# Kernel tuning notes

Hardware: AMD Instinct MI355X
Metric: run time of the kernel (lower is better)

Reference implementation:

```python
import jax, jax.numpy as jnp
import numpy as np

D_MODEL = 2048
D_INNER = 2 * D_MODEL      # expand=2
D_STATE = 16
D_CONV = 4
DT_RANK = D_MODEL // 16    # ceil(2048/16)=128
BATCH, SEQLEN = 2, 1024


def setup_inputs() -> dict:
    key = jax.random.key(0)
    ks = jax.random.split(key, 10)
    s = 0.02
    inp = {
        "hidden_states": jax.random.normal(ks[0], (BATCH, SEQLEN, D_MODEL), jnp.float32),
        "in_proj_w": jax.random.normal(ks[1], (2 * D_INNER, D_MODEL), jnp.float32) * s,
        "conv_w": jax.random.normal(ks[2], (D_INNER, D_CONV), jnp.float32) * s,
        "conv_b": jax.random.normal(ks[3], (D_INNER,), jnp.float32) * s,
        "x_proj_w": jax.random.normal(ks[4], (DT_RANK + 2 * D_STATE, D_INNER), jnp.float32) * s,
        "dt_proj_w": jax.random.normal(ks[5], (D_INNER, DT_RANK), jnp.float32) * s,
        "dt_proj_b": jax.random.normal(ks[6], (D_INNER,), jnp.float32) * 0.1,
        "A_log": jnp.log(jnp.tile(jnp.arange(1, D_STATE + 1, dtype=jnp.float32), (D_INNER, 1))),
        "D": jnp.ones((D_INNER,), jnp.float32),
        "out_proj_w": jax.random.normal(ks[7], (D_MODEL, D_INNER), jnp.float32) * s,
    }
    return inp


def _mamba_forward(hidden_states, in_proj_w, conv_w, conv_b, x_proj_w,
                   dt_proj_w, dt_proj_b, A_log, D, out_proj_w):
    B, L, _ = hidden_states.shape
    # input projection -> x, z  (each [B, L, D_INNER])
    xz = jnp.einsum('bld,ed->ble', hidden_states, in_proj_w)
    x, z = jnp.split(xz, 2, axis=-1)
    # causal depthwise conv1d (kernel D_CONV) + SiLU
    x_pad = jnp.pad(x, ((0, 0), (D_CONV - 1, 0), (0, 0)))
    windows = jnp.stack([x_pad[:, k:k + L, :] for k in range(D_CONV)], axis=-1)  # [B,L,D,K]
    x_conv = jnp.einsum('bldk,dk->bld', windows, conv_w) + conv_b
    x_act = jax.nn.silu(x_conv)
    # data-dependent SSM parameters
    x_dbl = jnp.einsum('bld,ed->ble', x_act, x_proj_w)
    dt, Bc, Cc = jnp.split(x_dbl, [DT_RANK, DT_RANK + D_STATE], axis=-1)
    dt = jax.nn.softplus(jnp.einsum('blr,dr->bld', dt, dt_proj_w) + dt_proj_b)  # [B,L,D_INNER]
    A = -jnp.exp(A_log)  # [D_INNER, D_STATE]

    # selective scan over time (carry h: [B, D_INNER, D_STATE])
    def step(h, inp):
        x_t, dt_t, B_t, C_t = inp  # [B,D],[B,D],[B,N],[B,N]
        dA = jnp.exp(dt_t[:, :, None] * A[None])          # [B,D,N]
        dBx = dt_t[:, :, None] * B_t[:, None, :] * x_t[:, :, None]
        h = h * dA + dBx
        y = jnp.einsum('bdn,bn->bd', h, C_t)
        return h, y

    xs = (x_act.transpose(1, 0, 2), dt.transpose(1, 0, 2),
          Bc.transpose(1, 0, 2), Cc.transpose(1, 0, 2))
    h0 = jnp.zeros((B, D_INNER, D_STATE), x_act.dtype)
    _, ys = jax.lax.scan(step, h0, xs)          # [L,B,D_INNER]
    y = ys.transpose(1, 0, 2) + x_act * D       # skip connection D*x
    y = y * jax.nn.silu(z)                      # gating
    return jnp.einsum('bld,md->blm', y, out_proj_w)


def reference(hidden_states, in_proj_w, conv_w, conv_b, x_proj_w,
              dt_proj_w, dt_proj_b, A_log, D, out_proj_w):
    return _mamba_forward(hidden_states, in_proj_w, conv_w, conv_b, x_proj_w,
                          dt_proj_w, dt_proj_b, A_log, D, out_proj_w)
```

## Files before the change

### kernel.cpp

```cpp
#include <hip/hip_runtime.h>
#include <cstdint>
#include <cstddef>

#define D_MODEL 2048
#define D_INNER 4096
#define D_IN2   8192
#define D_STATE 16
#define D_CONVK 4
#define DT_RANK 128
#define BATCH   2
#define SEQLEN  1024
#define BL      (BATCH*SEQLEN)
#define XDBL_N  (DT_RANK + 2*D_STATE)
#define XPW_NPAD 256
#define XPROJ_SPLITS 8
#define OUT_SPLITS 2

#define NCHUNK  16
#define LCHUNK  (SEQLEN/NCHUNK)
#define CHW     (BATCH*D_INNER*D_STATE)

#define NB_HID   2048
#define NB_IPW   8192
#define NB_XPW   320
#define NB_XPWZ  192
#define NB_DTW   256
#define NB_OPW   4096
#define NB_XDBLZ 320

typedef short  s8v  __attribute__((ext_vector_type(8)));
typedef float  f4v  __attribute__((ext_vector_type(4)));

__device__ __forceinline__ float softplus_f(float v) {
    return (v > 20.f) ? v : log1pf(__expf(v));
}
__device__ __forceinline__ float silu_f(float v) {
    return v / (1.f + __expf(-v));
}
__device__ __forceinline__ float bf2f(short s) {
    return __uint_as_float(((uint32_t)(uint16_t)s) << 16);
}
__device__ __forceinline__ uint16_t f2bf(float f) {
    uint32_t u = __float_as_uint(f);
    return (uint16_t)((u + 0x7FFFu + ((u >> 16) & 1u)) >> 16);
}
__device__ __forceinline__ uint32_t packbf(float lo, float hi) {
    return ((uint32_t)f2bf(hi) << 16) | (uint32_t)f2bf(lo);
}
__device__ __forceinline__ float quad_sum(float p) {
    p += __int_as_float(__builtin_amdgcn_update_dpp(
            0, __float_as_int(p), 0xB1, 0xF, 0xF, true));
    p += __int_as_float(__builtin_amdgcn_update_dpp(
            0, __float_as_int(p), 0x4E, 0xF, 0xF, true));
    return p;
}

#define GLD16(gp, lp)                                                          \
    __builtin_amdgcn_global_load_lds(                                          \
        (const __attribute__((address_space(1))) void*)(gp),                   \
        (__attribute__((address_space(3))) void*)(lp), 16, 0, 0)

__global__ __launch_bounds__(256)
void k_cast_all(const float* __restrict__ s0, uint32_t* __restrict__ d0,
                const float* __restrict__ s1, uint32_t* __restrict__ d1,
                const float* __restrict__ s2, uint32_t* __restrict__ d2,
                const float* __restrict__ s3, uint32_t* __restrict__ d3,
                const float* __restrict__ s4, uint32_t* __restrict__ d4,
                uint32_t* __restrict__ z0, uint32_t* __restrict__ z1)
{
    int blk = blockIdx.x;
    const float* src = nullptr; uint32_t* dst; int base; int zero = 0;
    if      (blk < NB_HID) { src = s0; dst = d0; base = blk; }
    else if ((blk -= NB_HID)  < NB_IPW)  { src = s1; dst = d1; base = blk; }
    else if ((blk -= NB_IPW)  < NB_XPW)  { src = s2; dst = d2; base = blk; }
    else if ((blk -= NB_XPW)  < NB_XPWZ) { dst = z0; base = blk; zero = 1; }
    else if ((blk -= NB_XPWZ) < NB_DTW)  { src = s3; dst = d3; base = blk; }
    else if ((blk -= NB_DTW)  < NB_OPW)  { src = s4; dst = d4; base = blk; }
    else                                 { dst = z1; base = blk - NB_OPW; zero = 1; }
    const int i = base * 256 + threadIdx.x;
    if (zero) { ((uint4*)dst)[i] = make_uint4(0u, 0u, 0u, 0u); return; }
    const float4 a = ((const float4*)src)[i * 2];
    const float4 b = ((const float4*)src)[i * 2 + 1];
    uint4 o;
    o.x = packbf(a.x, a.y); o.y = packbf(a.z, a.w);
    o.z = packbf(b.x, b.y); o.w = packbf(b.z, b.w);
    ((uint4*)dst)[i] = o;
}

template<int EPI>
__device__ __forceinline__
void gemm_body(const short* __restrict__ A, int lda,
               const short* __restrict__ W, int ldw,
               void* __restrict__ Cv, int ldc, int M, int kchunk)
{
    __shared__ short sA[128 * 64];
    __shared__ short sW[128 * 64];

    const int tid = threadIdx.x;
    const int w   = tid >> 6;
    const int L   = tid & 63;
    const int bm  = blockIdx.y * 128;
    const int bn  = blockIdx.x * 128;
    const int k0  = blockIdx.z * kchunk;

    const int rsub = L >> 3;
    const int c8   = (((L & 7) - rsub) & 7) * 8;
    const short* Ag[4]; const short* Wg[4];
#pragma unroll
    for (int j = 0; j < 4; j++) {
        Ag[j] = A + (size_t)(bm + w * 32 + j * 8 + rsub) * lda + c8 + k0;
        Wg[j] = W + (size_t)(bn + w * 32 + j * 8 + rsub) * ldw + c8 + k0;
    }

    const int wm = (w >> 1) * 64;
    const int wn = (w & 1) * 64;
    const int cl = L & 15;
    const int qd = L >> 4;

    f4v acc[4][4];
#pragma unroll
    for (int i = 0; i < 4; i++)
#pragma unroll
        for (int j = 0; j < 4; j++) acc[i][j] = (f4v){0.f, 0.f, 0.f, 0.f};

    for (int k = 0; k < kchunk; k += 64) {
#pragma unroll
        for (int j = 0; j < 4; j++)
            GLD16(Ag[j] + k, &sA[(w * 32 + j * 8) * 64]);
#pragma unroll
        for (int j = 0; j < 4; j++)
            GLD16(Wg[j] + k, &sW[(w * 32 + j * 8) * 64]);
        __syncthreads();
#pragma unroll
        for (int kk = 0; kk < 2; kk++) {
            const int sl = ((kk * 4 + qd + cl) & 7) * 8;
            s8v a[4], b[4];
#pragma unroll
            for (int mt = 0; mt < 4; mt++)
                a[mt] = *(const s8v*)&sA[(wm + mt * 16 + cl) * 64 + sl];
#pragma unroll
            for (int nt = 0; nt < 4; nt++)
                b[nt] = *(const s8v*)&sW[(wn + nt * 16 + cl) * 64 + sl];
#pragma unroll
            for (int mt = 0; mt < 4; mt++)
#pragma unroll
                for (int nt = 0; nt < 4; nt++)
                    acc[mt][nt] = __builtin_amdgcn_mfma_f32_16x16x32_bf16(
                        a[mt], b[nt], acc[mt][nt], 0, 0, 0);
        }
        __syncthreads();
    }

    float* Cf = (float*)Cv;
    if (EPI == 0) Cf += (size_t)blockIdx.z * M * ldc;
    short* Cs = (short*)Cv;
#pragma unroll
    for (int mt = 0; mt < 4; mt++) {
        const int row0 = bm + wm + mt * 16 + qd * 4;
#pragma unroll
        for (int nt = 0; nt < 4; nt++) {
            const int col = bn + wn + nt * 16 + cl;
            if (EPI == 3 && col >= XDBL_N) continue;
#pragma unroll
            for (int r = 0; r < 4; r++) {
                const float v = acc[mt][nt][r];
                if      (EPI == 2) Cs[(size_t)(row0 + r) * ldc + col] = (short)f2bf(v);
                else if (EPI == 3) atomicAdd(&Cf[(size_t)(row0 + r) * ldc + col], v);
                else               Cf[(size_t)(row0 + r) * ldc + col] = v;
            }
        }
    }
}

__global__ __launch_bounds__(256)
void k_gemm_inproj(const short* A, const short* W, short* C)
{ gemm_body<2>(A, D_MODEL, W, D_MODEL, C, D_IN2, BL, D_MODEL); }

__global__ __launch_bounds__(256)
void k_gemm_xproj(const short* A, const short* W, float* C)
{ gemm_body<3>(A, D_INNER, W, D_INNER, C, XDBL_N, BL, D_INNER / XPROJ_SPLITS); }

__global__ __launch_bounds__(256)
void k_gemm_outproj(const short* A, const short* W, float* C)
{ gemm_body<0>(A, D_INNER, W, D_INNER, C, D_MODEL, BL, D_INNER / OUT_SPLITS); }

__global__ __launch_bounds__(256)
void k_reduce_out(const float* __restrict__ P, float* __restrict__ out)
{
    const int i = blockIdx.x * 256 + threadIdx.x;
    const float4 a = ((const float4*)P)[i];
    const float4 b = ((const float4*)(P + (size_t)BL * D_MODEL))[i];
    ((float4*)out)[i] = make_float4(a.x + b.x, a.y + b.y, a.z + b.z, a.w + b.w);
}

__global__ __launch_bounds__(256)
void k_gemm_dt(const float* __restrict__ Af, const short* __restrict__ W,
               const float* __restrict__ bias, float* __restrict__ C)
{
    __shared__ short sA[2 * 128 * 64];
    __shared__ short sW[2 * 128 * 64];

    const int tid = threadIdx.x;
    const int w   = tid >> 6;
    const int L   = tid & 63;
    const int bm  = blockIdx.y * 128;
    const int bn  = blockIdx.x * 128;

#pragma unroll
    for (int ci = 0; ci < 8; ci++) {
        const int c_lin = tid * 8 + ci;
        const int r = c_lin >> 4;
        const int c = c_lin & 15;
        const float* src = Af + (size_t)(bm + r) * XDBL_N + c * 8;
        const float4 u = *(const float4*)src;
        const float4 v = *(const float4*)(src + 4);
        const int half = c >> 3, cc = c & 7;
        const int slot = (cc + r) & 7;
        uint4 o;
        o.x = packbf(u.x, u.y); o.y = packbf(u.z, u.w);
        o.z = packbf(v.x, v.y); o.w = packbf(v.z, v.w);
        *(uint4*)&sA[half * 8192 + r * 64 + slot * 8] = o;
    }
    const int rsub = L >> 3;
    const int c8   = (((L & 7) - rsub) & 7) * 8;
#pragma unroll
    for (int half = 0; half < 2; half++)
#pragma unroll
        for (int j = 0; j < 4; j++)
            GLD16(W + (size_t)(bn + w * 32 + j * 8 + rsub) * DT_RANK + half * 64 + c8,
                  &sW[half * 8192 + (w * 32 + j * 8) * 64]);
    __syncthreads();

    const int wm = (w >> 1) * 64;
    const int wn = (w & 1) * 64;
    const int cl = L & 15;
    const int qd = L >> 4;

    f4v acc[4][4];
#pragma unroll
    for (int i = 0; i < 4; i++)
#pragma unroll
        for (int j = 0; j < 4; j++) acc[i][j] = (f4v){0.f, 0.f, 0.f, 0.f};

#pragma unroll
    for (int ks = 0; ks < 4; ks++) {
        const int half = ks >> 1;
        const int sl = (((ks & 1) * 4 + qd + cl) & 7) * 8;
        s8v a[4], b[4];
#pragma unroll
        for (int mt = 0; mt < 4; mt++)
            a[mt] = *(const s8v*)&sA[half * 8192 + (wm + mt * 16 + cl) * 64 + sl];
#pragma unroll
        for (int nt = 0; nt < 4; nt++)
            b[nt] = *(const s8v*)&sW[half * 8192 + (wn + nt * 16 + cl) * 64 + sl];
#pragma unroll
        for (int mt = 0; mt < 4; mt++)
#pragma unroll
            for (int nt = 0; nt < 4; nt++)
                acc[mt][nt] = __builtin_amdgcn_mfma_f32_16x16x32_bf16(
                    a[mt], b[nt], acc[mt][nt], 0, 0, 0);
    }

#pragma unroll
    for (int mt = 0; mt < 4; mt++) {
        const int row0 = bm + wm + mt * 16 + qd * 4;
#pragma unroll
        for (int nt = 0; nt < 4; nt++) {
            const int col = bn + wn + nt * 16 + cl;
            const float bc = bias[col];
#pragma unroll
            for (int r = 0; r < 4; r++)
                C[(size_t)(row0 + r) * D_INNER + col] = softplus_f(acc[mt][nt][r] + bc);
        }
    }
}

__global__ __launch_bounds__(256)
void k_conv(const short* __restrict__ xz_bf, const float* __restrict__ cw,
            const float* __restrict__ cb, short* __restrict__ x_bf)
{
    const int idx = blockIdx.x * 256 + threadIdx.x;
    const int d  = idx & (D_INNER - 1);
    const int bl = idx >> 12;
    const int l  = bl & (SEQLEN - 1);
    const int b  = bl >> 10;
    const short* xb = xz_bf + (size_t)b * SEQLEN * D_IN2 + d;
    float acc = cb[d];
#pragma unroll
    for (int k = 0; k < D_CONVK; k++) {
        const int ll = l + k - (D_CONVK - 1);
        if (ll >= 0) acc = fmaf(bf2f(xb[(size_t)ll * D_IN2]), cw[d * D_CONVK + k], acc);
    }
    x_bf[idx] = (short)f2bf(silu_f(acc));
}

__global__ __launch_bounds__(256)
void k_scan_p1(const short* __restrict__ x_bf, const float* __restrict__ dt,
               const float* __restrict__ xdbl, const float* __restrict__ A_log,
               float* __restrict__ h_end, float* __restrict__ Pprod)
{
    const int c   = blockIdx.y;
    const int ch0 = blockIdx.x * 64;
    const int b   = ch0 >> 12;
    const int d0  = ch0 & (D_INNER - 1);
    const int tid = threadIdx.x;
    const int g   = tid >> 2;
    const int q   = tid & 3;
    const int d   = d0 + g;

    const float4 Al = *(const float4*)&A_log[(d << 4) + (q << 2)];
    float An[4] = {-__expf(Al.x), -__expf(Al.y), -__expf(Al.z), -__expf(Al.w)};
    float h[4]  = {0.f, 0.f, 0.f, 0.f};
    float Pp[4] = {1.f, 1.f, 1.f, 1.f};

    __shared__ float s_x [16][68];
    __shared__ float s_dt[16][68];
    __shared__ float s_B [16][20];

    const int lt  = tid >> 4;
    const int ld4 = (tid & 15) * 4;

    for (int sub = 0; sub < LCHUNK / 16; sub++) {
        const int l0 = c * LCHUNK + sub * 16;
        const size_t bl = (size_t)(b * SEQLEN + l0 + lt);
        __syncthreads();
        {
            const short4 sx = *(const short4*)&x_bf[bl * D_INNER + d0 + ld4];
            const float4 dv = *(const float4*)&dt[bl * D_INNER + d0 + ld4];
            *(float4*)&s_x [lt][ld4] =
                make_float4(bf2f(sx.x), bf2f(sx.y), bf2f(sx.z), bf2f(sx.w));
            *(float4*)&s_dt[lt][ld4] = dv;
            if (tid < 64) {
                const int t2 = tid >> 2, k = (tid & 3) * 4;
                const size_t bl2 = (size_t)(b * SEQLEN + l0 + t2);
                *(float4*)&s_B[t2][k] =
                    *(const float4*)&xdbl[bl2 * XDBL_N + DT_RANK + k];
            }
        }
        __syncthreads();
#pragma unroll
        for (int t = 0; t < 16; t++) {
            const float xv  = s_x [t][g];
            const float dtv = s_dt[t][g];
            const float4 Bq = *(const float4*)&s_B[t][q * 4];
            const float Bv[4] = {Bq.x, Bq.y, Bq.z, Bq.w};
            const float dtx = dtv * xv;
#pragma unroll
            for (int j = 0; j < 4; j++) {
                const float dA = __expf(dtv * An[j]);
                h[j]  = fmaf(h[j], dA, dtx * Bv[j]);
                Pp[j] *= dA;
            }
        }
    }
    const size_t i0 = (size_t)c * CHW + (((size_t)(b * D_INNER + d)) << 4) + (q << 2);
    *(float4*)&h_end[i0] = make_float4(h[0], h[1], h[2], h[3]);
    *(float4*)&Pprod[i0] = make_float4(Pp[0], Pp[1], Pp[2], Pp[3]);
}

__global__ __launch_bounds__(256)
void k_scan_p3(const short* __restrict__ x_bf, short* __restrict__ y_bf,
               const float* __restrict__ dt, const float* __restrict__ xdbl,
               const short* __restrict__ xz_bf, const float* __restrict__ A_log,
               const float* __restrict__ Dvec,
               const float* __restrict__ h_end, const float* __restrict__ Pbuf)
{
    const int c   = blockIdx.y;
    const int ch0 = blockIdx.x * 64;
    const int b   = ch0 >> 12;
    const int d0  = ch0 & (D_INNER - 1);
    const int tid = threadIdx.x;
    const int g   = tid >> 2;
    const int q   = tid & 3;
    const int d   = d0 + g;

    const float4 Al = *(const float4*)&A_log[(d << 4) + (q << 2)];
    float An[4] = {-__expf(Al.x), -__expf(Al.y), -__expf(Al.z), -__expf(Al.w)};
    const float Dd = Dvec[d];

    float h[4] = {0.f, 0.f, 0.f, 0.f};
    const size_t base = (((size_t)(b * D_INNER + d)) << 4) + (q << 2);
    for (int j = 0; j < c; j++) {
        const float4 he = *(const float4*)&h_end[(size_t)j * CHW + base];
        const float4 Pp = *(const float4*)&Pbuf [(size_t)j * CHW + base];
        h[0] = fmaf(Pp.x, h[0], he.x);
        h[1] = fmaf(Pp.y, h[1], he.y);
        h[2] = fmaf(Pp.z, h[2], he.z);
        h[3] = fmaf(Pp.w, h[3], he.w);
    }

    __shared__ float s_x [16][68];
    __shared__ float s_dt[16][68];
    __shared__ float s_z [16][68];
    __shared__ float s_B [16][20];
    __shared__ float s_C [16][20];

    const int lt  = tid >> 4;
    const int ld4 = (tid & 15) * 4;

    for (int sub = 0; sub < LCHUNK / 16; sub++) {
        const int l0 = c * LCHUNK + sub * 16;
        const size_t bl = (size_t)(b * SEQLEN + l0 + lt);
        __syncthreads();
        {
            const short4 sx = *(const short4*)&x_bf[bl * D_INNER + d0 + ld4];
            const float4 dv = *(const float4*)&dt[bl * D_INNER + d0 + ld4];
            const short4 zv = *(const short4*)&xz_bf[bl * D_IN2 + D_INNER + d0 + ld4];
            *(float4*)&s_x [lt][ld4] =
                make_float4(bf2f(sx.x), bf2f(sx.y), bf2f(sx.z), bf2f(sx.w));
            *(float4*)&s_dt[lt][ld4] = dv;
            *(float4*)&s_z [lt][ld4] =
                make_float4(bf2f(zv.x), bf2f(zv.y), bf2f(zv.z), bf2f(zv.w));
            if (tid < 128) {
                const int t2 = (tid & 63) >> 2, k = (tid & 3) * 4;
                const size_t bl2 = (size_t)(b * SEQLEN + l0 + t2);
                const int off = (tid < 64) ? 0 : D_STATE;
                const float4 v =
                    *(const float4*)&xdbl[bl2 * XDBL_N + DT_RANK + off + k];
                if (tid < 64) *(float4*)&s_B[t2][k] = v;
                else          *(float4*)&s_C[t2][k] = v;
            }
        }
        __syncthreads();
        const size_t orow = (size_t)(b * SEQLEN + l0);
#pragma unroll
        for (int t = 0; t < 16; t++) {
            const float xv  = s_x [t][g];
            const float dtv = s_dt[t][g];
            const float4 Bq = *(const float4*)&s_B[t][q * 4];
            const float4 Cq = *(const float4*)&s_C[t][q * 4];
            const float Bv[4] = {Bq.x, Bq.y, Bq.z, Bq.w};
            const float Cv[4] = {Cq.x, Cq.y, Cq.z, Cq.w};
            const float dtx = dtv * xv;
            float p = 0.f;
#pragma unroll
            for (int j = 0; j < 4; j++) {
                const float dA = __expf(dtv * An[j]);
                h[j] = fmaf(h[j], dA, dtx * Bv[j]);
                p = fmaf(h[j], Cv[j], p);
            }
            p = quad_sum(p);
            if (q == 0) {
                const float yv = fmaf(xv, Dd, p) * silu_f(s_z[t][g]);
                y_bf[(orow + t) * D_INNER + d] = (short)f2bf(yv);
            }
        }
    }
}

extern "C" void kernel_launch(void* const* d_in, const int* in_sizes, int n_in,
                              void* d_out, int out_size, void* d_ws, size_t ws_size,
                              hipStream_t stream)
{
    const float* hidden     = (const float*)d_in[0];
    const float* in_proj_w  = (const float*)d_in[1];
    const float* conv_w     = (const float*)d_in[2];
    const float* conv_b     = (const float*)d_in[3];
    const float* x_proj_w   = (const float*)d_in[4];
    const float* dt_proj_w  = (const float*)d_in[5];
    const float* dt_proj_b  = (const float*)d_in[6];
    const float* A_log      = (const float*)d_in[7];
    const float* Dvec       = (const float*)d_in[8];
    const float* out_proj_w = (const float*)d_in[9];
    float* out = (float*)d_out;

    const size_t MB = 1ull << 20;
    char* ws = (char*)d_ws;
    short* xz_bf   = (short*)(ws);
    short* x_bf    = (short*)(ws + 32 * MB);
    short* ipw_bf  = (short*)(ws + 48 * MB);
    short* y_bf    = (short*)(ws + 48 * MB);
    float* h_end   = (float*)(ws + 64 * MB);
    float* Pbuf    = (float*)(ws + 72 * MB);
    short* hid_bf  = (short*)(ws + 80 * MB);
    short* opw_bf  = (short*)(ws + 88 * MB);
    float* dt_f32  = (float*)(ws + 104 * MB);
    float* op_part = (float*)(ws + 104 * MB);
    short* xpw_bf  = (short*)(ws + 136 * MB);
    short* dtw_bf  = (short*)(ws + 138 * MB);
    float* xdbl_f  = (float*)(ws + 139 * MB);

    const dim3 blk(256);

    k_cast_all<<<dim3(NB_HID + NB_IPW + NB_XPW + NB_XPWZ + NB_DTW + NB_OPW + NB_XDBLZ),
                blk, 0, stream>>>(
        hidden, (uint32_t*)hid_bf, in_proj_w, (uint32_t*)ipw_bf,
        x_proj_w, (uint32_t*)xpw_bf, dt_proj_w, (uint32_t*)dtw_bf,
        out_proj_w, (uint32_t*)opw_bf,
        (uint32_t*)(xpw_bf + (size_t)XDBL_N * D_INNER),
        (uint32_t*)xdbl_f);

    k_gemm_inproj<<<dim3(D_IN2 / 128, BL / 128, 1), blk, 0, stream>>>(
        hid_bf, ipw_bf, xz_bf);

    k_conv<<<dim3((BL * D_INNER) / 256), blk, 0, stream>>>(
        xz_bf, conv_w, conv_b, x_bf);

    k_gemm_xproj<<<dim3(XPW_NPAD / 128, BL / 128, XPROJ_SPLITS), blk, 0, stream>>>(
        x_bf, xpw_bf, xdbl_f);

    k_gemm_dt<<<dim3(D_INNER / 128, BL / 128), blk, 0, stream>>>(
        xdbl_f, dtw_bf, dt_proj_b, dt_f32);

    k_scan_p1<<<dim3(BATCH * D_INNER / 64, NCHUNK - 1), blk, 0, stream>>>(
        x_bf, dt_f32, xdbl_f, A_log, h_end, Pbuf);
    k_scan_p3<<<dim3(BATCH * D_INNER / 64, NCHUNK), blk, 0, stream>>>(
        x_bf, y_bf, dt_f32, xdbl_f, xz_bf, A_log, Dvec, h_end, Pbuf);

    k_gemm_outproj<<<dim3(D_MODEL / 128, BL / 128, OUT_SPLITS), blk, 0, stream>>>(
        y_bf, opw_bf, op_part);
    k_reduce_out<<<dim3(BL * D_MODEL / 4 / 256), blk, 0, stream>>>(op_part, out);
}
```

Before: 450.8 us.

## Use 256x256-tile, 8-wave, 4-stage pipelined GEMM for in_proj

Replaces the 128x128 in_proj GEMM with a dedicated 256x256 tile kernel using 512 threads (8 waves), a 4-deep LDS ring buffer with direct global-to-LDS loads, swizzled LDS layout, and explicit vmcnt/barrier scheduling with setprio around MFMA bursts. Larger tiles raise arithmetic intensity and halve global operand traffic per FLOP; the deeper pipeline is meant to hide load latency. It risks fewer blocks (32x8=256) relative to CU count, high register pressure for 32 accumulators per thread, and 128KB LDS use limiting occupancy.

After: 556.6 us. +23.5%, slower.

```diff
diff --git a/kernel.cpp b/kernel.cpp
--- a/kernel.cpp
+++ b/kernel.cpp
@@ -172,9 +172,129 @@
     }
 }
 
-__global__ __launch_bounds__(256)
+template<int EPI>
+__device__ __forceinline__
+void gemm256_body(const short* __restrict__ A, int lda,
+                  const short* __restrict__ W, int ldw,
+                  void* __restrict__ Cv, int ldc, int kchunk)
+{
+    __shared__ short sA[4][256 * 32];
+    __shared__ short sB[4][256 * 32];
+
+    const int tid = threadIdx.x;
+    const int w   = tid >> 6;
+    const int L   = tid & 63;
+    const int bm  = blockIdx.y * 256;
+    const int bn  = blockIdx.x * 256;
+    const int k0  = blockIdx.z * kchunk;
+    const int NT  = kchunk >> 5;
+
+    const int srow = w * 16 + (L >> 2);
+    const int g    = ((L & 3) - (srow >> 1)) & 3;
+    const short* Ag = A + (size_t)(bm + srow) * lda + k0 + g * 8;
+    const short* Wg = W + (size_t)(bn + srow) * ldw + k0 + g * 8;
+    const int sbase = w * 512;
+
+    const int wm = w >> 2;
+    const int wn = w & 3;
+    const int cl = L & 15;
+    const int qd = L >> 4;
+    const int ra = wm * 128 + cl;
+    const int rb = wn * 64 + cl;
+    const int aoff = ra * 32 + ((qd + (ra >> 1)) & 3) * 8;
+    const int boff = rb * 32 + ((qd + (rb >> 1)) & 3) * 8;
+
+    f4v acc[8][4];
+#pragma unroll
+    for (int i = 0; i < 8; i++)
+#pragma unroll
+        for (int j = 0; j < 4; j++) acc[i][j] = (f4v){0.f, 0.f, 0.f, 0.f};
+
+#define STG(t_, rd_) do {                                                      \
+        GLD16(Ag + (size_t)(rd_) * 128 * lda + (t_) * 32,                      \
+              &sA[(t_) & 3][(rd_) * 4096 + sbase]);                            \
+        GLD16(Wg + (size_t)(rd_) * 128 * ldw + (t_) * 32,                      \
+              &sB[(t_) & 3][(rd_) * 4096 + sbase]);                            \
+    } while (0)
+
+#define MF(mt_, nt_, aa_, bb_)                                                 \
+    acc[mt_][nt_] = __builtin_amdgcn_mfma_f32_16x16x32_bf16(                   \
+        aa_, bb_, acc[mt_][nt_], 0, 0, 0)
+
+    STG(0, 0); STG(0, 1);
+    __builtin_amdgcn_sched_barrier(0);
+    STG(1, 0); STG(1, 1);
+    __builtin_amdgcn_sched_barrier(0);
+    STG(2, 0); STG(2, 1);
+    asm volatile("s_waitcnt vmcnt(8)" ::: "memory");
+    __builtin_amdgcn_s_barrier();
+
+#pragma unroll 4
+    for (int t = 0; t < NT; ++t) {
+        const short* pA = &sA[t & 3][0];
+        const short* pB = &sB[t & 3][0];
+
+        s8v a0 = *(const s8v*)(pA + aoff);
+        s8v a1 = *(const s8v*)(pA + aoff + 512);
+        s8v a2 = *(const s8v*)(pA + aoff + 1024);
+        s8v a3 = *(const s8v*)(pA + aoff + 1536);
+        s8v b0 = *(const s8v*)(pB + boff);
+        s8v b1 = *(const s8v*)(pB + boff + 512);
+        s8v b2 = *(const s8v*)(pB + boff + 1024);
+        s8v b3 = *(const s8v*)(pB + boff + 1536);
+        if (t + 3 < NT) STG(t + 3, 0);
+        __builtin_amdgcn_s_barrier();
+        asm volatile("s_waitcnt lgkmcnt(0)" ::: "memory");
+        __builtin_amdgcn_s_setprio(1);
+        MF(0, 0, a0, b0); MF(1, 0, a1, b0); MF(2, 0, a2, b0); MF(3, 0, a3, b0);
+        MF(0, 1, a0, b1); MF(1, 1, a1, b1); MF(2, 1, a2, b1); MF(3, 1, a3, b1);
+        MF(0, 2, a0, b2); MF(1, 2, a1, b2); MF(2, 2, a2, b2); MF(3, 2, a3, b2);
+        MF(0, 3, a0, b3); MF(1, 3, a1, b3); MF(2, 3, a2, b3); MF(3, 3, a3, b3);
+        __builtin_amdgcn_s_setprio(0);
+        __builtin_amdgcn_s_barrier();
+
+        a0 = *(const s8v*)(pA + aoff + 2048);
+        a1 = *(const s8v*)(pA + aoff + 2560);
+        a2 = *(const s8v*)(pA + aoff + 3072);
+        a3 = *(const s8v*)(pA + aoff + 3584);
+        if (t + 3 < NT) STG(t + 3, 1);
+        if      (t < NT - 3)  asm volatile("s_waitcnt vmcnt(8)" ::: "memory");
+        else if (t == NT - 3) asm volatile("s_waitcnt vmcnt(4)" ::: "memory");
+        else if (t == NT - 2) asm volatile("s_waitcnt vmcnt(0)" ::: "memory");
+        __builtin_amdgcn_s_barrier();
+        asm volatile("s_waitcnt lgkmcnt(0)" ::: "memory");
+        __builtin_amdgcn_s_setprio(1);
+        MF(4, 0, a0, b0); MF(5, 0, a1, b0); MF(6, 0, a2, b0); MF(7, 0, a3, b0);
+        MF(4, 1, a0, b1); MF(5, 1, a1, b1); MF(6, 1, a2, b1); MF(7, 1, a3, b1);
+        MF(4, 2, a0, b2); MF(5, 2, a1, b2); MF(6, 2, a2, b2); MF(7, 2, a3, b2);
+        MF(4, 3, a0, b3); MF(5, 3, a1, b3); MF(6, 3, a2, b3); MF(7, 3, a3, b3);
+        __builtin_amdgcn_s_setprio(0);
+        __builtin_amdgcn_s_barrier();
+    }
+#undef MF
+#undef STG
+
+    float* Cf = (float*)Cv;
+    short* Cs = (short*)Cv;
+#pragma unroll
+    for (int mt = 0; mt < 8; mt++) {
+        const int row0 = bm + wm * 128 + mt * 16 + qd * 4;
+#pragma unroll
+        for (int nt = 0; nt < 4; nt++) {
+            const int col = bn + wn * 64 + nt * 16 + cl;
+#pragma unroll
+            for (int r = 0; r < 4; r++) {
+                const float v = acc[mt][nt][r];
+                if (EPI == 2) Cs[(size_t)(row0 + r) * ldc + col] = (short)f2bf(v);
+                else          Cf[(size_t)(row0 + r) * ldc + col] = v;
+            }
+        }
+    }
+}
+
+__global__ __launch_bounds__(512, 2)
 void k_gemm_inproj(const short* A, const short* W, short* C)
-{ gemm_body<2>(A, D_MODEL, W, D_MODEL, C, D_IN2, BL, D_MODEL); }
+{ gemm256_body<2>(A, D_MODEL, W, D_MODEL, C, D_IN2, D_MODEL); }
 
 __global__ __launch_bounds__(256)
 void k_gemm_xproj(const short* A, const short* W, float* C)
@@ -490,7 +610,7 @@
         (uint32_t*)(xpw_bf + (size_t)XDBL_N * D_INNER),
         (uint32_t*)xdbl_f);
 
-    k_gemm_inproj<<<dim3(D_IN2 / 128, BL / 128, 1), blk, 0, stream>>>(
+    k_gemm_inproj<<<dim3(D_IN2 / 256, BL / 256, 1), dim3(512), 0, stream>>>(
         hid_bf, ipw_bf, xz_bf);
 
     k_conv<<<dim3((BL * D_INNER) / 256), blk, 0, stream>>>(
```

## Stage GEMM epilogues through LDS for coalesced stores; move dt softplus into scan

Applied to the files above, without the earlier changes.

The in_proj, out_proj and dt GEMM epilogues now write their accumulators to shared memory and then store them to global memory as coalesced 16-byte vectors, replacing the scattered per-element stores. The dt-projection bias add and softplus move out of the dt GEMM and into both scan kernels, so the GEMM writes raw values and the scans apply softplus when they load dt. The epilogues gain extra barriers and reuse LDS, and softplus is now computed twice, once in each scan pass.

New measurement: 461.1 us. +2.3%, slower.

```diff
diff --git a/kernel.cpp b/kernel.cpp
--- a/kernel.cpp
+++ b/kernel.cpp
@@ -93,8 +93,10 @@
                const short* __restrict__ W, int ldw,
                void* __restrict__ Cv, int ldc, int M, int kchunk)
 {
-    __shared__ short sA[128 * 64];
-    __shared__ short sW[128 * 64];
+    constexpr int SMEM_BYTES = (EPI == 2) ? 34816 : (EPI == 0) ? 33792 : 32768;
+    __shared__ __align__(16) char smem[SMEM_BYTES];
+    short* sA = (short*)smem;
+    short* sW = (short*)(smem + 16384);
 
     const int tid = threadIdx.x;
     const int w   = tid >> 6;
@@ -151,22 +153,64 @@
         __syncthreads();
     }
 
-    float* Cf = (float*)Cv;
-    if (EPI == 0) Cf += (size_t)blockIdx.z * M * ldc;
-    short* Cs = (short*)Cv;
-#pragma unroll
-    for (int mt = 0; mt < 4; mt++) {
-        const int row0 = bm + wm + mt * 16 + qd * 4;
-#pragma unroll
-        for (int nt = 0; nt < 4; nt++) {
-            const int col = bn + wn + nt * 16 + cl;
-            if (EPI == 3 && col >= XDBL_N) continue;
-#pragma unroll
-            for (int r = 0; r < 4; r++) {
-                const float v = acc[mt][nt][r];
-                if      (EPI == 2) Cs[(size_t)(row0 + r) * ldc + col] = (short)f2bf(v);
-                else if (EPI == 3) atomicAdd(&Cf[(size_t)(row0 + r) * ldc + col], v);
-                else               Cf[(size_t)(row0 + r) * ldc + col] = v;
+    if constexpr (EPI == 2) {
+        ushort (*sC)[136] = (ushort(*)[136])smem;
+        short* Cs = (short*)Cv;
+#pragma unroll
+        for (int mt = 0; mt < 4; mt++)
+#pragma unroll
+            for (int nt = 0; nt < 4; nt++)
+#pragma unroll
+                for (int r = 0; r < 4; r++)
+                    sC[wm + mt * 16 + qd * 4 + r][wn + nt * 16 + cl] =
+                        (ushort)f2bf(acc[mt][nt][r]);
+        __syncthreads();
+#pragma unroll
+        for (int it = 0; it < 8; it++) {
+            const int idx = it * 256 + tid;
+            const int row = idx >> 4;
+            const int c8s = (idx & 15) * 8;
+            *(uint4*)&Cs[(size_t)(bm + row) * ldc + bn + c8s] =
+                *(const uint4*)&sC[row][c8s];
+        }
+    } else if constexpr (EPI == 0) {
+        float (*sC)[132] = (float(*)[132])smem;
+        float* Cf = (float*)Cv + (size_t)blockIdx.z * M * ldc;
+#pragma unroll
+        for (int half = 0; half < 2; half++) {
+            __syncthreads();
+            if (wm == half * 64) {
+#pragma unroll
+                for (int mt = 0; mt < 4; mt++)
+#pragma unroll
+                    for (int nt = 0; nt < 4; nt++)
+#pragma unroll
+                        for (int r = 0; r < 4; r++)
+                            sC[mt * 16 + qd * 4 + r][wn + nt * 16 + cl] =
+                                acc[mt][nt][r];
+            }
+            __syncthreads();
+#pragma unroll
+            for (int it = 0; it < 8; it++) {
+                const int f4  = it * 256 + tid;
+                const int row = f4 >> 5;
+                const int c4  = (f4 & 31) * 4;
+                const float4 v = *(const float4*)&sC[row][c4];
+                *(float4*)&Cf[(size_t)(bm + half * 64 + row) * ldc + bn + c4] = v;
+            }
+        }
+    } else {
+        float* Cf = (float*)Cv;
+#pragma unroll
+        for (int mt = 0; mt < 4; mt++) {
+            const int row0 = bm + wm + mt * 16 + qd * 4;
+#pragma unroll
+            for (int nt = 0; nt < 4; nt++) {
+                const int col = bn + wn + nt * 16 + cl;
+                if (col >= XDBL_N) continue;
+#pragma unroll
+                for (int r = 0; r < 4; r++)
+                    atomicAdd(&Cf[(size_t)(row0 + r) * ldc + col], acc[mt][nt][r]);
             }
         }
     }
@@ -185,20 +229,12 @@
 { gemm_body<0>(A, D_INNER, W, D_INNER, C, D_MODEL, BL, D_INNER / OUT_SPLITS); }
 
 __global__ __launch_bounds__(256)
-void k_reduce_out(const float* __restrict__ P, float* __restrict__ out)
-{
-    const int i = blockIdx.x * 256 + threadIdx.x;
-    const float4 a = ((const float4*)P)[i];
-    const float4 b = ((const float4*)(P + (size_t)BL * D_MODEL))[i];
-    ((float4*)out)[i] = make_float4(a.x + b.x, a.y + b.y, a.z + b.z, a.w + b.w);
-}
-
-__global__ __launch_bounds__(256)
 void k_gemm_dt(const float* __restrict__ Af, const short* __restrict__ W,
-               const float* __restrict__ bias, float* __restrict__ C)
-{
-    __shared__ short sA[2 * 128 * 64];
-    __shared__ short sW[2 * 128 * 64];
+               float* __restrict__ C)
+{
+    __shared__ __align__(16) char smem[65536];
+    short* sA = (short*)smem;
+    short* sW = (short*)(smem + 32768);
 
     const int tid = threadIdx.x;
     const int w   = tid >> 6;
@@ -261,18 +297,40 @@
                     a[mt], b[nt], acc[mt][nt], 0, 0, 0);
     }
 
-#pragma unroll
-    for (int mt = 0; mt < 4; mt++) {
-        const int row0 = bm + wm + mt * 16 + qd * 4;
-#pragma unroll
-        for (int nt = 0; nt < 4; nt++) {
-            const int col = bn + wn + nt * 16 + cl;
-            const float bc = bias[col];
-#pragma unroll
-            for (int r = 0; r < 4; r++)
-                C[(size_t)(row0 + r) * D_INNER + col] = softplus_f(acc[mt][nt][r] + bc);
-        }
-    }
+    __syncthreads();
+    float (*sC)[132] = (float(*)[132])smem;
+#pragma unroll
+    for (int half = 0; half < 2; half++) {
+        __syncthreads();
+        if (wm == half * 64) {
+#pragma unroll
+            for (int mt = 0; mt < 4; mt++)
+#pragma unroll
+                for (int nt = 0; nt < 4; nt++)
+#pragma unroll
+                    for (int r = 0; r < 4; r++)
+                        sC[mt * 16 + qd * 4 + r][wn + nt * 16 + cl] =
+                            acc[mt][nt][r];
+        }
+        __syncthreads();
+#pragma unroll
+        for (int it = 0; it < 8; it++) {
+            const int f4  = it * 256 + tid;
+            const int row = f4 >> 5;
+            const int c4  = (f4 & 31) * 4;
+            const float4 v = *(const float4*)&sC[row][c4];
+            *(float4*)&C[(size_t)(bm + half * 64 + row) * D_INNER + bn + c4] = v;
+        }
+    }
+}
+
+__global__ __launch_bounds__(256)
+void k_reduce_out(const float* __restrict__ P, float* __restrict__ out)
+{
+    const int i = blockIdx.x * 256 + threadIdx.x;
+    const float4 a = ((const float4*)P)[i];
+    const float4 b = ((const float4*)(P + (size_t)BL * D_MODEL))[i];
+    ((float4*)out)[i] = make_float4(a.x + b.x, a.y + b.y, a.z + b.z, a.w + b.w);
 }
 
 __global__ __launch_bounds__(256)
@@ -295,8 +353,9 @@
 }
 
 __global__ __launch_bounds__(256)
-void k_scan_p1(const short* __restrict__ x_bf, const float* __restrict__ dt,
-               const float* __restrict__ xdbl, const float* __restrict__ A_log,
+void k_scan_p1(const short* __restrict__ x_bf, const float* __restrict__ dtr,
+               const float* __restrict__ dtb, const float* __restrict__ xdbl,
+               const float* __restrict__ A_log,
                float* __restrict__ h_end, float* __restrict__ Pprod)
 {
     const int c   = blockIdx.y;
@@ -319,6 +378,7 @@
 
     const int lt  = tid >> 4;
     const int ld4 = (tid & 15) * 4;
+    const float4 bb = *(const float4*)&dtb[d0 + ld4];
 
     for (int sub = 0; sub < LCHUNK / 16; sub++) {
         const int l0 = c * LCHUNK + sub * 16;
@@ -326,10 +386,12 @@
         __syncthreads();
         {
             const short4 sx = *(const short4*)&x_bf[bl * D_INNER + d0 + ld4];
-            const float4 dv = *(const float4*)&dt[bl * D_INNER + d0 + ld4];
+            const float4 dv = *(const float4*)&dtr[bl * D_INNER + d0 + ld4];
             *(float4*)&s_x [lt][ld4] =
                 make_float4(bf2f(sx.x), bf2f(sx.y), bf2f(sx.z), bf2f(sx.w));
-            *(float4*)&s_dt[lt][ld4] = dv;
+            *(float4*)&s_dt[lt][ld4] = make_float4(
+                softplus_f(dv.x + bb.x), softplus_f(dv.y + bb.y),
+                softplus_f(dv.z + bb.z), softplus_f(dv.w + bb.w));
             if (tid < 64) {
                 const int t2 = tid >> 2, k = (tid & 3) * 4;
                 const size_t bl2 = (size_t)(b * SEQLEN + l0 + t2);
@@ -360,7 +422,8 @@
 
 __global__ __launch_bounds__(256)
 void k_scan_p3(const short* __restrict__ x_bf, short* __restrict__ y_bf,
-               const float* __restrict__ dt, const float* __restrict__ xdbl,
+               const float* __restrict__ dtr, const float* __restrict__ dtb,
+               const float* __restrict__ xdbl,
                const short* __restrict__ xz_bf, const float* __restrict__ A_log,
                const float* __restrict__ Dvec,
                const float* __restrict__ h_end, const float* __restrict__ Pbuf)
@@ -397,6 +460,7 @@
 
     const int lt  = tid >> 4;
     const int ld4 = (tid & 15) * 4;
+    const float4 bb = *(const float4*)&dtb[d0 + ld4];
 
     for (int sub = 0; sub < LCHUNK / 16; sub++) {
         const int l0 = c * LCHUNK + sub * 16;
@@ -404,11 +468,13 @@
         __syncthreads();
         {
             const short4 sx = *(const short4*)&x_bf[bl * D_INNER + d0 + ld4];
-            const float4 dv = *(const float4*)&dt[bl * D_INNER + d0 + ld4];
+            const float4 dv = *(const float4*)&dtr[bl * D_INNER + d0 + ld4];
             const short4 zv = *(const short4*)&xz_bf[bl * D_IN2 + D_INNER + d0 + ld4];
             *(float4*)&s_x [lt][ld4] =
                 make_float4(bf2f(sx.x), bf2f(sx.y), bf2f(sx.z), bf2f(sx.w));
-            *(float4*)&s_dt[lt][ld4] = dv;
+            *(float4*)&s_dt[lt][ld4] = make_float4(
+                softplus_f(dv.x + bb.x), softplus_f(dv.y + bb.y),
+                softplus_f(dv.z + bb.z), softplus_f(dv.w + bb.w));
             *(float4*)&s_z [lt][ld4] =
                 make_float4(bf2f(zv.x), bf2f(zv.y), bf2f(zv.z), bf2f(zv.w));
             if (tid < 128) {
@@ -474,7 +540,7 @@
     float* Pbuf    = (float*)(ws + 72 * MB);
     short* hid_bf  = (short*)(ws + 80 * MB);
     short* opw_bf  = (short*)(ws + 88 * MB);
-    float* dt_f32  = (float*)(ws + 104 * MB);
+    float* dt_raw  = (float*)(ws + 104 * MB);
     float* op_part = (float*)(ws + 104 * MB);
     short* xpw_bf  = (short*)(ws + 136 * MB);
     short* dtw_bf  = (short*)(ws + 138 * MB);
@@ -500,12 +566,12 @@
         x_bf, xpw_bf, xdbl_f);
 
     k_gemm_dt<<<dim3(D_INNER / 128, BL / 128), blk, 0, stream>>>(
-        xdbl_f, dtw_bf, dt_proj_b, dt_f32);
+        xdbl_f, dtw_bf, dt_raw);
 
     k_scan_p1<<<dim3(BATCH * D_INNER / 64, NCHUNK - 1), blk, 0, stream>>>(
-        x_bf, dt_f32, xdbl_f, A_log, h_end, Pbuf);
+        x_bf, dt_raw, dt_proj_b, xdbl_f, A_log, h_end, Pbuf);
     k_scan_p3<<<dim3(BATCH * D_INNER / 64, NCHUNK), blk, 0, stream>>>(
-        x_bf, y_bf, dt_f32, xdbl_f, xz_bf, A_log, Dvec, h_end, Pbuf);
+        x_bf, y_bf, dt_raw, dt_proj_b, xdbl_f, xz_bf, A_log, Dvec, h_end, Pbuf);
 
     k_gemm_outproj<<<dim3(D_MODEL / 128, BL / 128, OUT_SPLITS), blk, 0, stream>>>(
         y_bf, opw_bf, op_part);
```
